# Performance work log

Measured on AMD Instinct MI355X. Metric: run time of the kernel, lower is better.

The kernel has to match this reference:

```python
import jax, jax.numpy as jnp
import numpy as np

NUM_MODES = 256
THRESHOLD = 1.0
ATAN_ALPHA = 2.0

@jax.custom_vjp
def atan_spike(u):
    # snntorch ATan surrogate: forward heaviside(u > 0)
    return (u > 0).astype(u.dtype)

def _atan_fwd(u):
    return atan_spike(u), u

def _atan_bwd(u, g):
    # grad = alpha/2 / (1 + (pi/2 * alpha * u)^2)
    return (g * (ATAN_ALPHA / 2.0) / (1.0 + (jnp.pi / 2.0 * ATAN_ALPHA * u) ** 2),)

atan_spike.defvjp(_atan_fwd, _atan_bwd)

def setup_inputs() -> dict:
    key = jax.random.key(0)
    k0, k1, k2, k3, k4 = jax.random.split(key, 5)
    B, N, P = 8192, 256, 32
    x = jax.random.normal(k0, (B, N), dtype=jnp.float32)
    W_lin = jax.random.normal(k1, (N, N), dtype=jnp.float32) * 0.05
    b_lin = jax.random.normal(k2, (N,), dtype=jnp.float32) * 0.05
    W_sel = jax.random.normal(k3, (P, NUM_MODES, N), dtype=jnp.float32) * 0.05
    b_sel = jax.random.normal(k4, (P, NUM_MODES), dtype=jnp.float32) * 0.05
    return {"x": x, "W_lin": W_lin, "b_lin": b_lin, "W_sel": W_sel, "b_sel": b_sel}

def reference(x, W_lin, b_lin, W_sel, b_sel):
    B = x.shape[0]
    # lin
    h = x @ W_lin.T + b_lin                       # [B, N]
    # regular Leaky, single step, mem=None: mem = beta*0 + h = h
    reg_mem = h
    reg_out = atan_spike(reg_mem - THRESHOLD)      # [B, N]
    # polymorphic neurons (vectorized over P):
    # mode selector scores: softmax over modes
    scores = jax.nn.softmax(jnp.einsum('bn,pmn->bpm', reg_out, W_sel) + b_sel, axis=-1)  # [B,P,M]
    # all NUM_MODES Leaky modes see mem=None -> mem = reg_out, identical spikes
    spk_mode = atan_spike(reg_out - THRESHOLD)     # [B, N] (N == NUM_MODES)
    # mixed = sum_i spk_i * scores = NUM_MODES * spk * scores (broadcast over mode/neuron axis)
    mixed = NUM_MODES * spk_mode[:, None, :] * scores  # [B, P, N]
    out = jnp.concatenate([reg_out, mixed.reshape(B, -1)], axis=-1)  # [B, N*(1+P)]
    return out
```

## Files before the change

### kernel.cpp

```cpp
#include <hip/hip_runtime.h>
#include <hip/hip_bf16.h>


#define SNN_B 8192
#define SNN_N 256
#define SNN_P 32
#define SNN_ROW (SNN_N * (SNN_P + 1))
#define BLK_ROWS 32

__global__ __launch_bounds__(256) void w_transpose_kernel(
    const float* __restrict__ W, float* __restrict__ WT)
{
    const int o = blockIdx.x * 256 + threadIdx.x;
    const int k = o >> 8, n = o & 255;
    WT[o] = W[n * SNN_N + k];
}

__global__ __launch_bounds__(256) void polysnn_main_kernel(
    const float* __restrict__ x,
    const float* __restrict__ W,
    const float* __restrict__ WT,
    const float* __restrict__ bias,
    float* __restrict__ out)
{
    __shared__ float xs[BLK_ROWS][SNN_N];

    const int tid  = threadIdx.x;
    const int lane = tid & 63;
    const int wave = tid >> 6;
    const int row0 = blockIdx.x * BLK_ROWS;

    {
        const float4* x4  = reinterpret_cast<const float4*>(x + (size_t)row0 * SNN_N);
        float4*       xsw = reinterpret_cast<float4*>(&xs[0][0]);
#pragma unroll
        for (int i = 0; i < 8; ++i) xsw[tid + i * 256] = x4[tid + i * 256];
    }
    __syncthreads();

    const int grow0 = row0 + wave * 8;
    const float4* wt4 = reinterpret_cast<const float4*>(WT);
    const float4* xs4 = reinterpret_cast<const float4*>(&xs[0][0]);
    const int xbase = wave * 8 * 64;

    float acc[8][4];
#pragma unroll
    for (int r = 0; r < 8; ++r)
#pragma unroll
        for (int c = 0; c < 4; ++c) acc[r][c] = 0.0f;

    float4 wcur0 = wt4[0 * 64 + lane];
    float4 wcur1 = wt4[1 * 64 + lane];
    float4 wcur2 = wt4[2 * 64 + lane];
    float4 wcur3 = wt4[3 * 64 + lane];
    float4 xcur[8];
#pragma unroll
    for (int r = 0; r < 8; ++r) xcur[r] = xs4[xbase + r * 64 + 0];

    float* const wfill = out + (size_t)grow0 * SNN_ROW;
    const float4 z = make_float4(0.f, 0.f, 0.f, 0.f);

    for (int i = 0; i < 64; ++i) {
        const int ip = (i + 1) & 63;
        float4 wnx0 = wt4[(ip * 4 + 0) * 64 + lane];
        float4 wnx1 = wt4[(ip * 4 + 1) * 64 + lane];
        float4 wnx2 = wt4[(ip * 4 + 2) * 64 + lane];
        float4 wnx3 = wt4[(ip * 4 + 3) * 64 + lane];
        float4 xnxt[8];
#pragma unroll
        for (int r = 0; r < 8; ++r) xnxt[r] = xs4[xbase + r * 64 + ip];

#pragma unroll
        for (int j = 0; j < 4; ++j) {
            const int fidx = ((i * 4 + j) << 6) + lane;
            const int rl   = fidx >> 11;
            const int c4   = fidx & 2047;
            *reinterpret_cast<float4*>(wfill + rl * SNN_ROW + SNN_N + (c4 << 2)) = z;
        }

#pragma unroll
        for (int r = 0; r < 8; ++r) {
            const float4 xr = xcur[r];
            acc[r][0] = fmaf(xr.x, wcur0.x, acc[r][0]);
            acc[r][1] = fmaf(xr.x, wcur0.y, acc[r][1]);
            acc[r][2] = fmaf(xr.x, wcur0.z, acc[r][2]);
            acc[r][3] = fmaf(xr.x, wcur0.w, acc[r][3]);
            acc[r][0] = fmaf(xr.y, wcur1.x, acc[r][0]);
            acc[r][1] = fmaf(xr.y, wcur1.y, acc[r][1]);
            acc[r][2] = fmaf(xr.y, wcur1.z, acc[r][2]);
            acc[r][3] = fmaf(xr.y, wcur1.w, acc[r][3]);
            acc[r][0] = fmaf(xr.z, wcur2.x, acc[r][0]);
            acc[r][1] = fmaf(xr.z, wcur2.y, acc[r][1]);
            acc[r][2] = fmaf(xr.z, wcur2.z, acc[r][2]);
            acc[r][3] = fmaf(xr.z, wcur2.w, acc[r][3]);
            acc[r][0] = fmaf(xr.w, wcur3.x, acc[r][0]);
            acc[r][1] = fmaf(xr.w, wcur3.y, acc[r][1]);
            acc[r][2] = fmaf(xr.w, wcur3.z, acc[r][2]);
            acc[r][3] = fmaf(xr.w, wcur3.w, acc[r][3]);
        }

        wcur0 = wnx0; wcur1 = wnx1; wcur2 = wnx2; wcur3 = wnx3;
#pragma unroll
        for (int r = 0; r < 8; ++r) xcur[r] = xnxt[r];
    }

    const float4 bb = reinterpret_cast<const float4*>(bias)[lane];
#pragma unroll
    for (int r = 0; r < 8; ++r) {
        float h[4] = {acc[r][0] + bb.x, acc[r][1] + bb.y,
                      acc[r][2] + bb.z, acc[r][3] + bb.w};
        float s[4];
#pragma unroll
        for (int c = 0; c < 4; ++c) {
            if (__builtin_expect(fabsf(h[c] - 1.0f) < 1e-3f, 0)) {
                const int n = 4 * lane + c;
                double a = (double)bias[n];
                const float* wr = W + (size_t)n * SNN_N;
                for (int k = 0; k < SNN_N; ++k)
                    a += (double)wr[k] * (double)xs[wave * 8 + r][k];
                s[c] = (a > 1.0) ? 1.0f : 0.0f;
            } else {
                s[c] = (h[c] > 1.0f) ? 1.0f : 0.0f;
            }
        }
        *reinterpret_cast<float4*>(out + (size_t)(grow0 + r) * SNN_ROW + (lane << 2))
            = make_float4(s[0], s[1], s[2], s[3]);
    }
}

__global__ __launch_bounds__(256) void polysnn_mono_kernel(
    const float* __restrict__ x, const float* __restrict__ W,
    const float* __restrict__ bias, float* __restrict__ out)
{
    __shared__ float xs[8][SNN_N];
    const int tid = threadIdx.x;
    const int row0 = blockIdx.x * 8;
    {
        const float4* x4  = reinterpret_cast<const float4*>(x + (size_t)row0 * SNN_N);
        float4*       xsw = reinterpret_cast<float4*>(&xs[0][0]);
        xsw[tid] = x4[tid]; xsw[tid + 256] = x4[tid + 256];
    }
    __syncthreads();
    const float4 zz = make_float4(0.f, 0.f, 0.f, 0.f);
#pragma unroll
    for (int r = 0; r < 8; ++r) {
        float4* o4 = reinterpret_cast<float4*>(out + (size_t)(row0 + r) * SNN_ROW + SNN_N);
#pragma unroll
        for (int i = 0; i < 8; ++i) o4[tid + i * 256] = zz;
    }
    const int n = tid;
    float acc[8];
#pragma unroll
    for (int r = 0; r < 8; ++r) acc[r] = 0.0f;
    const float4* w4  = reinterpret_cast<const float4*>(W + (size_t)n * SNN_N);
    const float4* xs4 = reinterpret_cast<const float4*>(&xs[0][0]);
#pragma unroll 4
    for (int k4 = 0; k4 < SNN_N / 4; ++k4) {
        const float4 w = w4[k4];
#pragma unroll
        for (int r = 0; r < 8; ++r) {
            const float4 xr = xs4[r * 64 + k4];
            acc[r] = fmaf(w.x, xr.x, acc[r]); acc[r] = fmaf(w.y, xr.y, acc[r]);
            acc[r] = fmaf(w.z, xr.z, acc[r]); acc[r] = fmaf(w.w, xr.w, acc[r]);
        }
    }
    const float bn = bias[n];
#pragma unroll
    for (int r = 0; r < 8; ++r) {
        const float h = acc[r] + bn;
        float spike;
        if (__builtin_expect(fabsf(h - 1.0f) < 1e-3f, 0)) {
            double a = (double)bn;
            const float* wr = W + (size_t)n * SNN_N;
            for (int k = 0; k < SNN_N; ++k) a += (double)wr[k] * (double)xs[r][k];
            spike = (a > 1.0) ? 1.0f : 0.0f;
        } else spike = (h > 1.0f) ? 1.0f : 0.0f;
        out[(size_t)(row0 + r) * SNN_ROW + n] = spike;
    }
}

extern "C" void kernel_launch(void* const* d_in, const int* in_sizes, int n_in,
                              void* d_out, int out_size, void* d_ws, size_t ws_size,
                              hipStream_t stream) {
    const float* x     = (const float*)d_in[0];
    const float* W_lin = (const float*)d_in[1];
    const float* b_lin = (const float*)d_in[2];
    float* out = (float*)d_out;

    if (ws_size >= (size_t)SNN_N * SNN_N * sizeof(float)) {
        float* WT = (float*)d_ws;
        w_transpose_kernel<<<256, 256, 0, stream>>>(W_lin, WT);
        polysnn_main_kernel<<<SNN_B / BLK_ROWS, 256, 0, stream>>>(x, W_lin, WT, b_lin, out);
    } else {
        polysnn_mono_kernel<<<SNN_B / 8, 256, 0, stream>>>(x, W_lin, b_lin, out);
    }
}
```

Before: 65.87 us.

## Move zero-fill of mixed output into transpose kernel and deepen W prefetch

```diff
diff --git a/kernel.cpp b/kernel.cpp
--- a/kernel.cpp
+++ b/kernel.cpp
@@ -8,15 +8,25 @@
 #define SNN_ROW (SNN_N * (SNN_P + 1))
 #define BLK_ROWS 32
 
-__global__ __launch_bounds__(256) void w_transpose_kernel(
-    const float* __restrict__ W, float* __restrict__ WT)
+__global__ __launch_bounds__(256) void fill_wt_kernel(
+    const float* __restrict__ W, float* __restrict__ WT,
+    float* __restrict__ out)
 {
-    const int o = blockIdx.x * 256 + threadIdx.x;
-    const int k = o >> 8, n = o & 255;
-    WT[o] = W[n * SNN_N + k];
-}
-
-__global__ __launch_bounds__(256) void polysnn_main_kernel(
+    const int b   = blockIdx.x;
+    const int tid = threadIdx.x;
+    if (b < SNN_B) {
+        float4* o4 = reinterpret_cast<float4*>(out + (size_t)b * SNN_ROW + SNN_N);
+        const float4 z = make_float4(0.f, 0.f, 0.f, 0.f);
+#pragma unroll
+        for (int i = 0; i < 8; ++i) o4[tid + i * 256] = z;
+    } else {
+        const int o = (b - SNN_B) * 256 + tid;
+        const int k = o >> 8, n = o & 255;
+        WT[o] = W[n * SNN_N + k];
+    }
+}
+
+__global__ __launch_bounds__(256) void polysnn_gemm_kernel(
     const float* __restrict__ x,
     const float* __restrict__ W,
     const float* __restrict__ WT,
@@ -49,60 +59,60 @@
 #pragma unroll
         for (int c = 0; c < 4; ++c) acc[r][c] = 0.0f;
 
-    float4 wcur0 = wt4[0 * 64 + lane];
-    float4 wcur1 = wt4[1 * 64 + lane];
-    float4 wcur2 = wt4[2 * 64 + lane];
-    float4 wcur3 = wt4[3 * 64 + lane];
-    float4 xcur[8];
-#pragma unroll
-    for (int r = 0; r < 8; ++r) xcur[r] = xs4[xbase + r * 64 + 0];
-
-    float* const wfill = out + (size_t)grow0 * SNN_ROW;
-    const float4 z = make_float4(0.f, 0.f, 0.f, 0.f);
-
-    for (int i = 0; i < 64; ++i) {
-        const int ip = (i + 1) & 63;
-        float4 wnx0 = wt4[(ip * 4 + 0) * 64 + lane];
-        float4 wnx1 = wt4[(ip * 4 + 1) * 64 + lane];
-        float4 wnx2 = wt4[(ip * 4 + 2) * 64 + lane];
-        float4 wnx3 = wt4[(ip * 4 + 3) * 64 + lane];
-        float4 xnxt[8];
-#pragma unroll
-        for (int r = 0; r < 8; ++r) xnxt[r] = xs4[xbase + r * 64 + ip];
-
-#pragma unroll
-        for (int j = 0; j < 4; ++j) {
-            const int fidx = ((i * 4 + j) << 6) + lane;
-            const int rl   = fidx >> 11;
-            const int c4   = fidx & 2047;
-            *reinterpret_cast<float4*>(wfill + rl * SNN_ROW + SNN_N + (c4 << 2)) = z;
-        }
-
-#pragma unroll
-        for (int r = 0; r < 8; ++r) {
-            const float4 xr = xcur[r];
-            acc[r][0] = fmaf(xr.x, wcur0.x, acc[r][0]);
-            acc[r][1] = fmaf(xr.x, wcur0.y, acc[r][1]);
-            acc[r][2] = fmaf(xr.x, wcur0.z, acc[r][2]);
-            acc[r][3] = fmaf(xr.x, wcur0.w, acc[r][3]);
-            acc[r][0] = fmaf(xr.y, wcur1.x, acc[r][0]);
-            acc[r][1] = fmaf(xr.y, wcur1.y, acc[r][1]);
-            acc[r][2] = fmaf(xr.y, wcur1.z, acc[r][2]);
-            acc[r][3] = fmaf(xr.y, wcur1.w, acc[r][3]);
-            acc[r][0] = fmaf(xr.z, wcur2.x, acc[r][0]);
-            acc[r][1] = fmaf(xr.z, wcur2.y, acc[r][1]);
-            acc[r][2] = fmaf(xr.z, wcur2.z, acc[r][2]);
-            acc[r][3] = fmaf(xr.z, wcur2.w, acc[r][3]);
-            acc[r][0] = fmaf(xr.w, wcur3.x, acc[r][0]);
-            acc[r][1] = fmaf(xr.w, wcur3.y, acc[r][1]);
-            acc[r][2] = fmaf(xr.w, wcur3.z, acc[r][2]);
-            acc[r][3] = fmaf(xr.w, wcur3.w, acc[r][3]);
-        }
-
-        wcur0 = wnx0; wcur1 = wnx1; wcur2 = wnx2; wcur3 = wnx3;
-#pragma unroll
-        for (int r = 0; r < 8; ++r) xcur[r] = xnxt[r];
-    }
+    float4 wA0 = wt4[(0 * 4 + 0) * 64 + lane];
+    float4 wA1 = wt4[(0 * 4 + 1) * 64 + lane];
+    float4 wA2 = wt4[(0 * 4 + 2) * 64 + lane];
+    float4 wA3 = wt4[(0 * 4 + 3) * 64 + lane];
+    float4 wB0 = wt4[(1 * 4 + 0) * 64 + lane];
+    float4 wB1 = wt4[(1 * 4 + 1) * 64 + lane];
+    float4 wB2 = wt4[(1 * 4 + 2) * 64 + lane];
+    float4 wB3 = wt4[(1 * 4 + 3) * 64 + lane];
+
+#define SNN_FMA_ITER(W0, W1, W2, W3, IT)                                 \
+    do {                                                                 \
+        _Pragma("unroll")                                                \
+        for (int r = 0; r < 8; ++r) {                                    \
+            const float4 xr = xs4[xbase + r * 64 + (IT)];                \
+            acc[r][0] = fmaf(xr.x, W0.x, acc[r][0]);                     \
+            acc[r][1] = fmaf(xr.x, W0.y, acc[r][1]);                     \
+            acc[r][2] = fmaf(xr.x, W0.z, acc[r][2]);                     \
+            acc[r][3] = fmaf(xr.x, W0.w, acc[r][3]);                     \
+            acc[r][0] = fmaf(xr.y, W1.x, acc[r][0]);                     \
+            acc[r][1] = fmaf(xr.y, W1.y, acc[r][1]);                     \
+            acc[r][2] = fmaf(xr.y, W1.z, acc[r][2]);                     \
+            acc[r][3] = fmaf(xr.y, W1.w, acc[r][3]);                     \
+            acc[r][0] = fmaf(xr.z, W2.x, acc[r][0]);                     \
+            acc[r][1] = fmaf(xr.z, W2.y, acc[r][1]);                     \
+            acc[r][2] = fmaf(xr.z, W2.z, acc[r][2]);                     \
+            acc[r][3] = fmaf(xr.z, W2.w, acc[r][3]);                     \
+            acc[r][0] = fmaf(xr.w, W3.x, acc[r][0]);                     \
+            acc[r][1] = fmaf(xr.w, W3.y, acc[r][1]);                     \
+            acc[r][2] = fmaf(xr.w, W3.z, acc[r][2]);                     \
+            acc[r][3] = fmaf(xr.w, W3.w, acc[r][3]);                     \
+        }                                                                \
+    } while (0)
+
+    for (int body = 0; body < 32; ++body) {
+        const int i0  = body * 2;
+        const int ipA = (i0 + 2) & 63;
+        const int ipB = (i0 + 3) & 63;
+
+        float4 tA0 = wt4[(ipA * 4 + 0) * 64 + lane];
+        float4 tA1 = wt4[(ipA * 4 + 1) * 64 + lane];
+        float4 tA2 = wt4[(ipA * 4 + 2) * 64 + lane];
+        float4 tA3 = wt4[(ipA * 4 + 3) * 64 + lane];
+        float4 tB0 = wt4[(ipB * 4 + 0) * 64 + lane];
+        float4 tB1 = wt4[(ipB * 4 + 1) * 64 + lane];
+        float4 tB2 = wt4[(ipB * 4 + 2) * 64 + lane];
+        float4 tB3 = wt4[(ipB * 4 + 3) * 64 + lane];
+
+        SNN_FMA_ITER(wA0, wA1, wA2, wA3, i0);
+        SNN_FMA_ITER(wB0, wB1, wB2, wB3, i0 + 1);
+
+        wA0 = tA0; wA1 = tA1; wA2 = tA2; wA3 = tA3;
+        wB0 = tB0; wB1 = tB1; wB2 = tB2; wB3 = tB3;
+    }
+#undef SNN_FMA_ITER
 
     const float4 bb = reinterpret_cast<const float4*>(bias)[lane];
 #pragma unroll
@@ -189,8 +199,8 @@
 
     if (ws_size >= (size_t)SNN_N * SNN_N * sizeof(float)) {
         float* WT = (float*)d_ws;
-        w_transpose_kernel<<<256, 256, 0, stream>>>(W_lin, WT);
-        polysnn_main_kernel<<<SNN_B / BLK_ROWS, 256, 0, stream>>>(x, W_lin, WT, b_lin, out);
+        fill_wt_kernel<<<SNN_B + 256, 256, 0, stream>>>(W_lin, WT, out);
+        polysnn_gemm_kernel<<<SNN_B / BLK_ROWS, 256, 0, stream>>>(x, W_lin, WT, b_lin, out);
     } else {
         polysnn_mono_kernel<<<SNN_B / 8, 256, 0, stream>>>(x, W_lin, b_lin, out);
     }
```

Measured after the change: 80.99 us. 22.9% more time.
